# Kernel optimization log

Hardware: AMD Instinct MI355X
Metric: run time of the kernel (lower is better)

The kernel has to match this reference:

```python
import jax, jax.numpy as jnp
import numpy as np

B, S, D, H = 2, 2048, 1024, 16
HD = D // H
SCALE = HD ** -0.5


def setup_inputs() -> dict:
    key = jax.random.key(0)
    k1, k2, k3 = jax.random.split(key, 3)
    x = jax.random.normal(k1, (B, S, D), dtype=jnp.float32)
    # causal mask: True = masked (as used by masked_fill)
    mask = jnp.triu(jnp.ones((S, S), dtype=bool), k=1)
    w_qkv = jax.random.normal(k2, (D, 3 * D), dtype=jnp.float32) * (D ** -0.5)
    b_qkv = jnp.zeros((3 * D,), dtype=jnp.float32)
    w_out = jax.random.normal(k3, (D, D), dtype=jnp.float32) * (D ** -0.5)
    b_out = jnp.zeros((D,), dtype=jnp.float32)
    return {"x": x, "mask": mask, "w_qkv": w_qkv, "b_qkv": b_qkv,
            "w_out": w_out, "b_out": b_out}


def reference(x, mask, w_qkv, b_qkv, w_out, b_out):
    # qkv projection and split
    qkv = x @ w_qkv + b_qkv                     # [b, s, 3D]
    q, k, v = jnp.split(qkv, 3, axis=-1)
    # b s (h d) -> b h s d
    def to_heads(t):
        return t.reshape(B, S, H, HD).transpose(0, 2, 1, 3)
    q, k, v = to_heads(q), to_heads(k), to_heads(v)
    # attention scores [b, h, s, s]
    scores = jnp.einsum('bhqd,bhkd->bhqk', q, k) * SCALE
    scores = jnp.where(mask, -jnp.inf, scores)
    attn = jax.nn.softmax(scores, axis=-1)      # dropout is identity (eval)
    out = jnp.einsum('bhqk,bhkd->bhqd', attn, v)
    out = out.transpose(0, 2, 1, 3).reshape(B, S, D)  # b h s d -> b s (h d)
    out = out @ w_out + b_out                   # out dropout identity (eval)
    return (out, k, v)
```

## Files before the change

### kernel.cpp

```cpp
#include <hip/hip_runtime.h>
#include <hip/hip_bf16.h>

typedef short bf16x8 __attribute__((ext_vector_type(8)));
typedef short u16x4v __attribute__((ext_vector_type(4)));
typedef float f32x4  __attribute__((ext_vector_type(4)));
typedef unsigned short u16;
typedef unsigned int   u32;

#define NB   2
#define NS   2048
#define ND   1024
#define NH   16
#define NHD  64
#define N3   3072
#define NM   4096

__device__ __forceinline__ u16 f2bf(float f) {
    u32 u;
    __builtin_memcpy(&u, &f, 4);
    u += 0x7fffu + ((u >> 16) & 1u);
    return (u16)(u >> 16);
}
__device__ __forceinline__ u16 f2bfn(float f) {
    __hip_bfloat16 h = __float2bfloat16(f);
    u16 r;
    __builtin_memcpy(&r, &h, 2);
    return r;
}
__device__ __forceinline__ bf16x8 load8f(const float* f) {
    float4 a = *(const float4*)f;
    float4 b = *(const float4*)(f + 4);
    bf16x8 r;
    r[0] = (short)f2bf(a.x); r[1] = (short)f2bf(a.y);
    r[2] = (short)f2bf(a.z); r[3] = (short)f2bf(a.w);
    r[4] = (short)f2bf(b.x); r[5] = (short)f2bf(b.y);
    r[6] = (short)f2bf(b.z); r[7] = (short)f2bf(b.w);
    return r;
}
__device__ __forceinline__ void gload_lds16(const void* g, void* l) {
    __builtin_amdgcn_global_load_lds(
        (const __attribute__((address_space(1))) u32*)g,
        (__attribute__((address_space(3))) u32*)l, 16, 0, 0);
}
__device__ __forceinline__ float hexp2(float x) {
    return __builtin_amdgcn_exp2f(x);
}

__global__ __launch_bounds__(256) void prep_cvt(
    const float* __restrict__ X, u16* __restrict__ Xb,
    const float* __restrict__ Wqkv, u16* __restrict__ WqkvT,
    const float* __restrict__ Wout, u16* __restrict__ WoutT)
{
    __shared__ float t[32][33];
    const int b = blockIdx.x;
    if (b < 2048) {
        const int i = (b * 256 + threadIdx.x) * 8;
        *(bf16x8*)(Xb + i) = load8f(X + i);
        return;
    }
    const float* in; u16* outp; int R, C, tIdx;
    if (b < 5120) { in = Wqkv; outp = WqkvT; R = ND; C = N3; tIdx = b - 2048; }
    else          { in = Wout; outp = WoutT; R = ND; C = ND; tIdx = b - 5120; }
    const int nbc = C >> 5;
    const int r0 = (tIdx / nbc) << 5;
    const int c0 = (tIdx % nbc) << 5;
    const int tr = threadIdx.x >> 3, tc = (threadIdx.x & 7) << 2;
    const float4 v = *(const float4*)(in + (size_t)(r0 + tr) * C + c0 + tc);
    t[tr][tc] = v.x; t[tr][tc + 1] = v.y; t[tr][tc + 2] = v.z; t[tr][tc + 3] = v.w;
    __syncthreads();
    u16x4v ov;
    ov[0] = (short)f2bf(t[tc + 0][tr]); ov[1] = (short)f2bf(t[tc + 1][tr]);
    ov[2] = (short)f2bf(t[tc + 2][tr]); ov[3] = (short)f2bf(t[tc + 3][tr]);
    *(u16x4v*)(outp + (size_t)(c0 + tr) * R + r0 + tc) = ov;
}

template<bool BF>
__global__ __launch_bounds__(256) void qkv_gemm(
    const float* __restrict__ Xf, const u16* __restrict__ Xb,
    const float* __restrict__ Wf, const u16* __restrict__ WbT,
    const float* __restrict__ bias,
    u16* __restrict__ q_ws, u16* __restrict__ vT_ws, u16* __restrict__ k_ws,
    float* __restrict__ k_out, float* __restrict__ v_out)
{
    __shared__ __align__(16) u16 SH[16384];
    u16* const Abase = SH;
    u16* const Bbase = SH + 8192;

    const int bm = blockIdx.x & 31;
    const int bn = blockIdx.x >> 5;
    const int m0 = bm * 128, n0 = bn * 128;
    const int tid = threadIdx.x;
    const int lane = tid & 63, wv = tid >> 6;
    const int wm = wv >> 1, wn = wv & 1;
    const int li = lane & 15, lg = lane >> 4;
    const int rowi = lane >> 2;
    const int gsw = (((lane & 3) ^ ((lane >> 2) & 3)) << 4);

    f32x4 acc[4][4];
    #pragma unroll
    for (int i = 0; i < 4; ++i)
        #pragma unroll
        for (int j = 0; j < 4; ++j)
            acc[i][j] = (f32x4){0.f, 0.f, 0.f, 0.f};

    auto stage = [&](int B, int k0) {
        u16* As_ = Abase + B * 4096;
        u16* Bs_ = Bbase + B * 4096;
        if constexpr (BF) {
            #pragma unroll
            for (int i = 0; i < 2; ++i) {
                const int r0 = wv * 32 + i * 16;
                gload_lds16((const char*)(Xb  + (size_t)(m0 + r0 + rowi) * ND + k0) + gsw, &As_[r0 * 32]);
                gload_lds16((const char*)(WbT + (size_t)(n0 + r0 + rowi) * ND + k0) + gsw, &Bs_[r0 * 32]);
            }
        } else {
            #pragma unroll
            for (int i = 0; i < 2; ++i) {
                const int e = tid * 16 + i * 8;
                const int row = e >> 5, col = e & 31;
                bf16x8 v = load8f(Xf + (size_t)(m0 + row) * ND + k0 + col);
                *(bf16x8*)(&As_[row * 32 + (((col >> 3) ^ (row & 3)) << 3)]) = v;
            }
            #pragma unroll
            for (int i = 0; i < 2; ++i) {
                const int krow = (tid >> 4) + 16 * i, ncol = (tid & 15) * 8;
                bf16x8 bv = load8f(Wf + (size_t)(k0 + krow) * N3 + n0 + ncol);
                #pragma unroll
                for (int jj = 0; jj < 8; ++jj) {
                    const int n_ = ncol + jj;
                    Bs_[n_ * 32 + ((((krow >> 3) ^ (n_ & 3)) << 3) | (krow & 7))] = (u16)bv[jj];
                }
            }
        }
    };

    stage(0, 0);
    __syncthreads();

    int buf = 0;
    for (int k0 = 0; k0 < ND; k0 += 32) {
        if (k0 + 32 < ND) stage(buf ^ 1, k0 + 32);

        const u16* As_ = Abase + buf * 4096;
        const u16* Bs_ = Bbase + buf * 4096;
        bf16x8 a[4], b[4];
        #pragma unroll
        for (int i = 0; i < 4; ++i) {
            const int row = wm * 64 + i * 16 + li;
            a[i] = *(const bf16x8*)(&As_[row * 32 + ((lg ^ (row & 3)) << 3)]);
        }
        #pragma unroll
        for (int j = 0; j < 4; ++j) {
            const int row = wn * 64 + j * 16 + li;
            b[j] = *(const bf16x8*)(&Bs_[row * 32 + ((lg ^ (row & 3)) << 3)]);
        }
        __builtin_amdgcn_s_setprio(1);
        #pragma unroll
        for (int i = 0; i < 4; ++i)
            #pragma unroll
            for (int j = 0; j < 4; ++j)
                acc[i][j] = __builtin_amdgcn_mfma_f32_16x16x32_bf16(a[i], b[j], acc[i][j], 0, 0, 0);
        __builtin_amdgcn_s_setprio(0);

        __syncthreads();
        buf ^= 1;
    }

    const int cls = bn >> 3;
    if (cls == 2) {
        u16* SM = SH;
        #pragma unroll
        for (int i = 0; i < 4; ++i) {
          #pragma unroll
          for (int j = 0; j < 4; ++j) {
            const int gn = n0 + wn * 64 + j * 16 + li;
            const float bval = bias[gn];
            const int c = gn & 1023, h = c >> 6, d = c & 63;
            const int n_ = wn * 64 + j * 16 + li;
            #pragma unroll
            for (int r = 0; r < 4; ++r) {
                const int gm = m0 + wm * 64 + i * 16 + lg * 4 + r;
                const int b_ = gm >> 11, sI = gm & 2047;
                const float v = acc[i][j][r] + bval;
                __builtin_nontemporal_store(v,
                    &v_out[(((size_t)(b_ * NH + h)) * NS + sI) * NHD + d]);
                const int m_ = wm * 64 + i * 16 + lg * 4 + r;
                SM[n_ * 128 + (m_ ^ ((n_ & 7) << 3))] = f2bfn(v);
            }
          }
        }
        __syncthreads();
        const int nrow = tid >> 1, mh = tid & 1;
        const int cdx = (n0 - 2048) + nrow;
        const int hh = cdx >> 6, d = cdx & 63;
        const int b_ = m0 >> 11;
        const int s0 = (m0 & 2047) + mh * 64;
        u16* dst = vT_ws + (((size_t)(b_ * NH + hh)) * NHD + d) * NS + s0;
        #pragma unroll
        for (int c8 = 0; c8 < 8; ++c8) {
            const int m_ = mh * 64 + c8 * 8;
            *(bf16x8*)(dst + c8 * 8) =
                *(const bf16x8*)(&SM[nrow * 128 + (m_ ^ ((nrow & 7) << 3))]);
        }
    } else {
        #pragma unroll
        for (int i = 0; i < 4; ++i) {
          #pragma unroll
          for (int j = 0; j < 4; ++j) {
            const int gn = n0 + wn * 64 + j * 16 + li;
            const float bval = bias[gn];
            const int c = gn & 1023, h = c >> 6, d = c & 63;
            #pragma unroll
            for (int r = 0; r < 4; ++r) {
                const int gm = m0 + wm * 64 + i * 16 + lg * 4 + r;
                const int b_ = gm >> 11, sI = gm & 2047;
                const float v = acc[i][j][r] + bval;
                const size_t hidx = (((size_t)(b_ * NH + h)) * NS + sI) * NHD + d;
                if (cls == 0) {
                    q_ws[hidx] = f2bfn(v * 0.18033688011112042f);
                } else {
                    __builtin_nontemporal_store(v, &k_out[hidx]);
                    k_ws[hidx] = f2bfn(v);
                }
            }
          }
        }
    }
}

__global__ __launch_bounds__(256, 4) void attn_fwd(
    u16* __restrict__ q_all, const u16* __restrict__ k_all,
    const u16* __restrict__ vT)
{
    __shared__ __align__(16) u16 Ks[2][64 * 64];
    __shared__ __align__(16) u16 Vs[2][64 * 64];
    __shared__ __align__(16) u16 Pl[4][16 * 64];

    const int tid = threadIdx.x;
    const int wv = tid >> 6, lane = tid & 63;
    const int li = lane & 15, lg = lane >> 4;
    const int bid = blockIdx.x;
    const int xcd = bid & 7, j = bid >> 3;
    const int bh  = (xcd << 2) | (j >> 5);
    const int jj  = j & 31;
    const int qt  = (j & 32) ? (31 - jj) : jj;
    const int q0  = qt * 64 + wv * 16;
    const int ntiles = qt + 1;

    u16* qp = q_all + (size_t)bh * NS * NHD;
    const u16* kp = k_all + (size_t)bh * NS * NHD;
    const u16* vp = vT + (size_t)bh * NHD * NS;

    const int rl = lane >> 3;
    const int gsw = ((lane & 7) * 16) ^ (rl << 4);
    const int rs = (li & 7) << 3;

    bf16x8 aq0 = *(const bf16x8*)(qp + (size_t)(q0 + li) * NHD + lg * 8);
    bf16x8 aq1 = *(const bf16x8*)(qp + (size_t)(q0 + li) * NHD + 32 + lg * 8);

    f32x4 o[4], ls;
    ls = (f32x4){0.f, 0.f, 0.f, 0.f};
    #pragma unroll
    for (int nf = 0; nf < 4; ++nf) o[nf] = (f32x4){0.f, 0.f, 0.f, 0.f};
    float m = 5.75f;

    const short onb = (short)0x3F80;
    const bf16x8 ones = {onb, onb, onb, onb, onb, onb, onb, onb};

    #define STAGE(B, KB) do {                                                           \
        _Pragma("unroll")                                                               \
        for (int i_ = 0; i_ < 2; ++i_) {                                                \
            const int row_ = 16 * wv + 8 * i_;                                          \
            gload_lds16((const char*)(kp + (size_t)((KB) + row_ + rl) * NHD) + gsw,     \
                        &Ks[B][row_ * 64]);                                             \
            gload_lds16((const char*)(vp + (size_t)(row_ + rl) * NS + (KB)) + gsw,      \
                        &Vs[B][row_ * 64]);                                             \
        } } while (0)

    STAGE(0, 0);
    __syncthreads();

    int buf = 0;
    for (int kt = 0; kt < ntiles; ++kt) {
        const int kb = kt * 64;
        if (kt + 1 < ntiles) STAGE(buf ^ 1, kb + 64);

        const u16* K = Ks[buf];
        const u16* V = Vs[buf];

        f32x4 s[4];
        __builtin_amdgcn_s_setprio(1);
        #pragma unroll
        for (int kq = 0; kq < 4; ++kq) {
            const u16* Kr = K + (kq * 16 + li) * 64;
            const bf16x8 b0 = *(const bf16x8*)(Kr + ((lg * 8) ^ rs));
            const bf16x8 b1 = *(const bf16x8*)(Kr + ((lg * 8 + 32) ^ rs));
            f32x4 t = (f32x4){0.f, 0.f, 0.f, 0.f};
            t = __builtin_amdgcn_mfma_f32_16x16x32_bf16(aq0, b0, t, 0, 0, 0);
            s[kq] = __builtin_amdgcn_mfma_f32_16x16x32_bf16(aq1, b1, t, 0, 0, 0);
        }
        __builtin_amdgcn_s_setprio(0);

        float mx = s[0][0];
        #pragma unroll
        for (int kq = 0; kq < 4; ++kq)
            #pragma unroll
            for (int r = 0; r < 4; ++r)
                mx = fmaxf(mx, s[kq][r]);
        if (__any(mx > m)) {
            #pragma unroll
            for (int dd = 1; dd < 64; dd <<= 1)
                mx = fmaxf(mx, __shfl_xor(mx, dd, 64));
            const float corr = hexp2(m - mx);
            m = mx;
            #pragma unroll
            for (int nf = 0; nf < 4; ++nf)
                #pragma unroll
                for (int r = 0; r < 4; ++r) o[nf][r] *= corr;
            #pragma unroll
            for (int r = 0; r < 4; ++r) ls[r] *= corr;
        }

        bf16x8 vf[4][2];
        #pragma unroll
        for (int nf = 0; nf < 4; ++nf) {
            const u16* Vr = V + (nf * 16 + li) * 64;
            vf[nf][0] = *(const bf16x8*)(Vr + ((lg * 8) ^ rs));
            vf[nf][1] = *(const bf16x8*)(Vr + ((lg * 8 + 32) ^ rs));
        }

        const bool maskt = (kt == ntiles - 1);
        u16* PW = Pl[wv];
        #pragma unroll
        for (int r = 0; r < 4; ++r) {
            const int q_ = lg * 4 + r;
            const int qrow = q0 + q_;
            const int qm = q_ & 7;
            #pragma unroll
            for (int kq = 0; kq < 4; ++kq) {
                float ev = hexp2(s[kq][r] - m);
                if (maskt && (kb + kq * 16 + li > qrow)) ev = 0.f;
                PW[q_ * 64 + ((((2 * kq + (li >> 3)) ^ qm) << 3) | (li & 7))] = f2bfn(ev);
            }
        }
        asm volatile("s_waitcnt lgkmcnt(0)" ::: "memory");
        const bf16x8 pa0 = *(const bf16x8*)(PW + li * 64 + ((lg ^ (li & 7)) << 3));
        const bf16x8 pa1 = *(const bf16x8*)(PW + li * 64 + (((lg + 4) ^ (li & 7)) << 3));
        __builtin_amdgcn_s_setprio(1);
        #pragma unroll
        for (int nf = 0; nf < 4; ++nf) {
            f32x4 t = __builtin_amdgcn_mfma_f32_16x16x32_bf16(pa0, vf[nf][0], o[nf], 0, 0, 0);
            o[nf] = __builtin_amdgcn_mfma_f32_16x16x32_bf16(pa1, vf[nf][1], t, 0, 0, 0);
        }
        ls = __builtin_amdgcn_mfma_f32_16x16x32_bf16(pa0, ones, ls, 0, 0, 0);
        ls = __builtin_amdgcn_mfma_f32_16x16x32_bf16(pa1, ones, ls, 0, 0, 0);
        __builtin_amdgcn_s_setprio(0);

        __syncthreads();
        buf ^= 1;
    }

    #pragma unroll
    for (int nf = 0; nf < 4; ++nf)
        #pragma unroll
        for (int r = 0; r < 4; ++r)
            qp[(size_t)(q0 + lg * 4 + r) * NHD + nf * 16 + li] = f2bfn(o[nf][r] / ls[r]);
    #undef STAGE
}

template<bool BF>
__global__ __launch_bounds__(256) void out_gemm(
    const u16* __restrict__ Aq,
    const float* __restrict__ Wf, const u16* __restrict__ WbT,
    const float* __restrict__ bias, float* __restrict__ outp)
{
    __shared__ __align__(16) u16 As[2][128 * 64];
    __shared__ __align__(16) u16 Bs[2][128 * 64];

    const int bm = blockIdx.x & 31;
    const int bn = blockIdx.x >> 5;
    const int m0 = bm * 128, n0 = bn * 128;
    const int tid = threadIdx.x;
    const int lane = tid & 63, wv = tid >> 6;
    const int wm = wv >> 1, wn = wv & 1;
    const int li = lane & 15, lg = lane >> 4;
    const int gsw = ((lane & 7) * 16) ^ ((lane >> 3) << 4);
    const int rsw = (li & 7) << 3;

    f32x4 acc[4][4];
    #pragma unroll
    for (int i = 0; i < 4; ++i)
        #pragma unroll
        for (int j = 0; j < 4; ++j)
            acc[i][j] = (f32x4){0.f, 0.f, 0.f, 0.f};

    auto stage = [&](int B, int k0) {
        const int h = k0 >> 6;
        #pragma unroll
        for (int i = 0; i < 4; ++i) {
            const int r0 = (i * 4 + wv) * 8;
            const int gm = m0 + r0 + (lane >> 3);
            const int b_ = gm >> 11, sI = gm & 2047;
            gload_lds16((const char*)(Aq + (((size_t)(b_ * NH + h)) * NS + sI) * NHD) + gsw,
                        &As[B][r0 * 64]);
            if constexpr (BF)
                gload_lds16((const char*)(WbT + (size_t)(n0 + r0 + (lane >> 3)) * ND + k0) + gsw,
                            &Bs[B][r0 * 64]);
        }
        if constexpr (!BF) {
            #pragma unroll
            for (int i = 0; i < 4; ++i) {
                const int krow = 16 * i + (tid >> 4), ncol = (tid & 15) * 8;
                bf16x8 bv = load8f(Wf + (size_t)(k0 + krow) * ND + n0 + ncol);
                #pragma unroll
                for (int jj = 0; jj < 8; ++jj) {
                    const int n_ = ncol + jj;
                    Bs[B][n_ * 64 + ((((krow >> 3) ^ (n_ & 7)) << 3) | (krow & 7))] = (u16)bv[jj];
                }
            }
        }
    };

    stage(0, 0);
    __syncthreads();

    int buf = 0;
    for (int k0 = 0; k0 < ND; k0 += 64) {
        if (k0 + 64 < ND) stage(buf ^ 1, k0 + 64);

        bf16x8 a[4][2], b[4][2];
        #pragma unroll
        for (int i = 0; i < 4; ++i)
            #pragma unroll
            for (int kk = 0; kk < 2; ++kk)
                a[i][kk] = *(const bf16x8*)(&As[buf][(wm * 64 + i * 16 + li) * 64 + ((kk * 32 + lg * 8) ^ rsw)]);
        #pragma unroll
        for (int j = 0; j < 4; ++j)
            #pragma unroll
            for (int kk = 0; kk < 2; ++kk)
                b[j][kk] = *(const bf16x8*)(&Bs[buf][(wn * 64 + j * 16 + li) * 64 + ((kk * 32 + lg * 8) ^ rsw)]);
        __builtin_amdgcn_s_setprio(1);
        #pragma unroll
        for (int i = 0; i < 4; ++i)
            #pragma unroll
            for (int j = 0; j < 4; ++j) {
                acc[i][j] = __builtin_amdgcn_mfma_f32_16x16x32_bf16(a[i][0], b[j][0], acc[i][j], 0, 0, 0);
                acc[i][j] = __builtin_amdgcn_mfma_f32_16x16x32_bf16(a[i][1], b[j][1], acc[i][j], 0, 0, 0);
            }
        __builtin_amdgcn_s_setprio(0);

        __syncthreads();
        buf ^= 1;
    }

    #pragma unroll
    for (int i = 0; i < 4; ++i) {
      #pragma unroll
      for (int j = 0; j < 4; ++j) {
        const int gn = n0 + wn * 64 + j * 16 + li;
        const float bval = bias[gn];
        #pragma unroll
        for (int r = 0; r < 4; ++r) {
            const int gm = m0 + wm * 64 + i * 16 + lg * 4 + r;
            __builtin_nontemporal_store(acc[i][j][r] + bval, &outp[(size_t)gm * ND + gn]);
        }
      }
    }
}

extern "C" void kernel_launch(void* const* d_in, const int* in_sizes, int n_in,
                              void* d_out, int out_size, void* d_ws, size_t ws_size,
                              hipStream_t stream)
{
    const float* X    = (const float*)d_in[0];
    const float* Wqkv = (const float*)d_in[2];
    const float* bqkv = (const float*)d_in[3];
    const float* Wout = (const float*)d_in[4];
    const float* bout = (const float*)d_in[5];

    const size_t HE = (size_t)NB * NH * NS * NHD;

    float* out  = (float*)d_out;
    float* kout = out + HE;
    float* vout = kout + HE;

    u16* q_ws  = (u16*)d_ws;
    u16* vT_ws = q_ws + HE;
    u16* k_ws  = vT_ws + HE;

    u16* Xb     = k_ws + HE;
    u16* WqkvT  = Xb + (size_t)NM * ND;
    u16* WoutT  = WqkvT + (size_t)ND * N3;
    const bool big = ws_size >= (size_t)41943040;

    if (big) {
        prep_cvt<<<dim3(6144), dim3(256), 0, stream>>>(X, Xb, Wqkv, WqkvT, Wout, WoutT);
        qkv_gemm<true><<<dim3(32 * 24), dim3(256), 0, stream>>>(
            X, Xb, Wqkv, WqkvT, bqkv, q_ws, vT_ws, k_ws, kout, vout);
    } else {
        qkv_gemm<false><<<dim3(32 * 24), dim3(256), 0, stream>>>(
            X, Xb, Wqkv, WqkvT, bqkv, q_ws, vT_ws, k_ws, kout, vout);
    }

    attn_fwd<<<dim3(1024), dim3(256), 0, stream>>>(q_ws, k_ws, vT_ws);

    if (big) {
        out_gemm<true><<<dim3(32 * 8), dim3(256), 0, stream>>>(
            q_ws, Wout, WoutT, bout, out);
    } else {
        out_gemm<false><<<dim3(32 * 8), dim3(256), 0, stream>>>(
            q_ws, Wout, WoutT, bout, out);
    }
}
```

Before: 113.6 us.

## Defer the P·V MFMAs to the next iteration to overlap with QK and softmax

The attention loop is software-pipelined. P and the V fragments for tile kt are held in registers, and their P·V and row-sum MFMAs run in iteration kt+1 right after the QK MFMAs, with a final drain after the loop. The online-softmax rescale is still applied after the deferred accumulation, so the result stays mathematically equivalent. The aim is to let the matrix work overlap the exp, max and LDS-write phase and so hide latency. The cost is more live registers, which could lower occupancy or cause spills.

```diff
diff --git a/kernel.cpp b/kernel.cpp
--- a/kernel.cpp
+++ b/kernel.cpp
@@ -267,6 +267,9 @@
     const short onb = (short)0x3F80;
     const bf16x8 ones = {onb, onb, onb, onb, onb, onb, onb, onb};
 
+    bf16x8 Ppa0, Ppa1;
+    bf16x8 Pvf[4][2];
+
     #define STAGE(B, KB) do {                                                           \
         _Pragma("unroll")                                                               \
         for (int i_ = 0; i_ < 2; ++i_) {                                                \
@@ -299,6 +302,15 @@
             t = __builtin_amdgcn_mfma_f32_16x16x32_bf16(aq0, b0, t, 0, 0, 0);
             s[kq] = __builtin_amdgcn_mfma_f32_16x16x32_bf16(aq1, b1, t, 0, 0, 0);
         }
+        if (kt > 0) {
+            #pragma unroll
+            for (int nf = 0; nf < 4; ++nf) {
+                f32x4 t = __builtin_amdgcn_mfma_f32_16x16x32_bf16(Ppa0, Pvf[nf][0], o[nf], 0, 0, 0);
+                o[nf] = __builtin_amdgcn_mfma_f32_16x16x32_bf16(Ppa1, Pvf[nf][1], t, 0, 0, 0);
+            }
+            ls = __builtin_amdgcn_mfma_f32_16x16x32_bf16(Ppa0, ones, ls, 0, 0, 0);
+            ls = __builtin_amdgcn_mfma_f32_16x16x32_bf16(Ppa1, ones, ls, 0, 0, 0);
+        }
         __builtin_amdgcn_s_setprio(0);
 
         float mx = s[0][0];
@@ -321,12 +333,11 @@
             for (int r = 0; r < 4; ++r) ls[r] *= corr;
         }
 
-        bf16x8 vf[4][2];
         #pragma unroll
         for (int nf = 0; nf < 4; ++nf) {
             const u16* Vr = V + (nf * 16 + li) * 64;
-            vf[nf][0] = *(const bf16x8*)(Vr + ((lg * 8) ^ rs));
-            vf[nf][1] = *(const bf16x8*)(Vr + ((lg * 8 + 32) ^ rs));
+            Pvf[nf][0] = *(const bf16x8*)(Vr + ((lg * 8) ^ rs));
+            Pvf[nf][1] = *(const bf16x8*)(Vr + ((lg * 8 + 32) ^ rs));
         }
 
         const bool maskt = (kt == ntiles - 1);
@@ -344,21 +355,21 @@
             }
         }
         asm volatile("s_waitcnt lgkmcnt(0)" ::: "memory");
-        const bf16x8 pa0 = *(const bf16x8*)(PW + li * 64 + ((lg ^ (li & 7)) << 3));
-        const bf16x8 pa1 = *(const bf16x8*)(PW + li * 64 + (((lg + 4) ^ (li & 7)) << 3));
-        __builtin_amdgcn_s_setprio(1);
-        #pragma unroll
-        for (int nf = 0; nf < 4; ++nf) {
-            f32x4 t = __builtin_amdgcn_mfma_f32_16x16x32_bf16(pa0, vf[nf][0], o[nf], 0, 0, 0);
-            o[nf] = __builtin_amdgcn_mfma_f32_16x16x32_bf16(pa1, vf[nf][1], t, 0, 0, 0);
-        }
-        ls = __builtin_amdgcn_mfma_f32_16x16x32_bf16(pa0, ones, ls, 0, 0, 0);
-        ls = __builtin_amdgcn_mfma_f32_16x16x32_bf16(pa1, ones, ls, 0, 0, 0);
-        __builtin_amdgcn_s_setprio(0);
+        Ppa0 = *(const bf16x8*)(PW + li * 64 + ((lg ^ (li & 7)) << 3));
+        Ppa1 = *(const bf16x8*)(PW + li * 64 + (((lg + 4) ^ (li & 7)) << 3));
+        asm volatile("s_waitcnt lgkmcnt(0)" ::: "memory");
 
         __syncthreads();
         buf ^= 1;
     }
+
+    #pragma unroll
+    for (int nf = 0; nf < 4; ++nf) {
+        f32x4 t = __builtin_amdgcn_mfma_f32_16x16x32_bf16(Ppa0, Pvf[nf][0], o[nf], 0, 0, 0);
+        o[nf] = __builtin_amdgcn_mfma_f32_16x16x32_bf16(Ppa1, Pvf[nf][1], t, 0, 0, 0);
+    }
+    ls = __builtin_amdgcn_mfma_f32_16x16x32_bf16(Ppa0, ones, ls, 0, 0, 0);
+    ls = __builtin_amdgcn_mfma_f32_16x16x32_bf16(Ppa1, ones, ls, 0, 0, 0);
 
     #pragma unroll
     for (int nf = 0; nf < 4; ++nf)
```

Result: slower. 122.8 us (+8.1%).
